# Optimization experiments

Measured on AMD Instinct MI355X. Metric: run time of the kernel, lower is better.

The kernel has to match this reference:

```python
import jax, jax.numpy as jnp
import numpy as np

DT = 5e-05
NUM_SUBSTEPS = 100
SPRING_Y = 30000.0
DASHPOT_DAMPING = 100.0
DRAG_DAMPING = 1.0
N_VERTICES = 100000
N_SPRINGS = 1000000


def setup_inputs() -> dict:
    key = jax.random.key(0)
    k1, k2, k3, k4 = jax.random.split(key, 4)
    x = jax.random.normal(k1, (N_VERTICES, 3), dtype=jnp.float32)
    x = x.at[:, 2].add(3.0)  # start mostly above the ground plane z=0
    # spring endpoints, guaranteed distinct so rest length / norm is never 0
    idx1 = jax.random.randint(k2, (N_SPRINGS,), 0, N_VERTICES)
    off = jax.random.randint(k3, (N_SPRINGS,), 1, N_VERTICES)
    idx2 = (idx1 + off) % N_VERTICES
    springs = jnp.stack([idx1, idx2], axis=1).astype(jnp.int64)
    # rest lengths = initial spring lengths (realistic: starts near equilibrium)
    rest = jnp.linalg.norm(x[idx2] - x[idx1], axis=1).astype(jnp.float32)
    masses = jax.random.uniform(k4, (N_VERTICES,), jnp.float32, 0.5, 1.5)
    return {
        "init_vertices": x,
        "init_springs": springs,
        "init_rest_lengths": rest,
        "init_masses": masses,
    }


def reference(init_vertices, init_springs, init_rest_lengths, init_masses):
    idx1 = init_springs[:, 0]
    idx2 = init_springs[:, 1]
    masses = init_masses[:, None]                      # [V,1]
    rest = init_rest_lengths[:, None]                  # [S,1]
    gravity = jnp.array([0.0, 0.0, -9.8], dtype=init_vertices.dtype)
    drag = jnp.exp(jnp.asarray(-DT * DRAG_DAMPING, dtype=init_vertices.dtype))

    def substep(carry, _):
        x, v = carry
        dis = x[idx2] - x[idx1]                        # [S,3] gather
        length = jnp.linalg.norm(dis, axis=1, keepdims=True)
        d = dis / length                               # unit spring direction
        spring_f = SPRING_Y * (length / rest - 1.0) * d
        v_rel = jnp.sum((v[idx2] - v[idx1]) * d, axis=1, keepdims=True)
        f_pair = spring_f + DASHPOT_DAMPING * v_rel * d  # fused spring+dashpot
        forces = masses * gravity                      # [V,3]
        forces = forces.at[idx1].add(f_pair)           # scatter-add
        forces = forces.at[idx2].add(-f_pair)
        v = (v + DT * forces / masses) * drag          # explicit Euler + drag
        x = x + DT * v
        x = x.at[:, 2].set(jnp.maximum(x[:, 2], 0.0))  # ground clamp
        v = v.at[:, 2].set(jnp.where(x[:, 2] == 0.0, 0.0, v[:, 2]))
        return (x, v), None

    v0 = jnp.zeros_like(init_vertices)
    (x, v), _ = jax.lax.scan(substep, (init_vertices, v0), None, length=NUM_SUBSTEPS)
    return x
```

## Files before the change

kernel.cpp:

```cpp
#include <hip/hip_runtime.h>
#include <hip/hip_fp16.h>

#define DT 5e-5f
#define SPRING_Y 30000.0f
#define DASHPOT 100.0f
#define DRAG 0.9999500012499792f



__global__ void init_k(const float* __restrict__ x0, float4* __restrict__ xv,
                       int* __restrict__ deg, int nv) {
    int i = blockIdx.x * blockDim.x + threadIdx.x;
    if (i < nv) {
        xv[2 * i]     = make_float4(x0[3 * i], x0[3 * i + 1], x0[3 * i + 2], 0.0f);
        xv[2 * i + 1] = make_float4(0.0f, 0.0f, 0.0f, 0.0f);
        deg[i] = 0;
    }
}

__global__ void fill_sliced_k(const int2* __restrict__ springs,
                              const float* __restrict__ rest,
                              int* __restrict__ deg, unsigned* __restrict__ adj,
                              int ns, int nv, int S) {
    int b = blockIdx.x;
    int slice = b & 7;
    int s = (b >> 3) * blockDim.x + threadIdx.x;
    if (s >= ns) return;

    int lo = (int)(((long long)slice * nv) >> 3);
    int hi = (int)(((long long)(slice + 1) * nv) >> 3);

    int2 p = springs[s];
    unsigned h = __half_as_ushort(__float2half(1.0f / rest[s])) & 0x7fffu;
    if (p.x >= lo && p.x < hi) {
        int a = atomicAdd(&deg[p.x], 1);
        adj[p.x * S + a] = ((unsigned)p.y << 15) | h;
    }
    if (p.y >= lo && p.y < hi) {
        int c = atomicAdd(&deg[p.y], 1);
        adj[p.y * S + c] = ((unsigned)p.x << 15) | h;
    }
}


__device__ __forceinline__ void spring_accum(
        int par, unsigned e, float msk, float4 t1, float4 t2,
        const float4& xa, const float4& va,
        float& fx, float& fy, float& fz) {
    float invr = __uint_as_float(((e & 0x7fffu) << 13) + (112u << 23));
    float4 xb, u;
    xb.x = par ? t2.x : t1.x;
    xb.y = par ? t2.y : t1.y;
    xb.z = par ? t2.z : t1.z;
    u.x  = par ? t1.x : t2.x;
    u.y  = par ? t1.y : t2.y;
    u.z  = par ? t1.z : t2.z;
    float vbx = __shfl_xor(u.x, 1);
    float vby = __shfl_xor(u.y, 1);
    float vbz = __shfl_xor(u.z, 1);

    float dx = xb.x - xa.x, dy = xb.y - xa.y, dz = xb.z - xa.z;
    float len = sqrtf(dx * dx + dy * dy + dz * dz);
    float il = 1.0f / len;
    float ddx = dx * il, ddy = dy * il, ddz = dz * il;
    float vrel = (vbx - va.x) * ddx + (vby - va.y) * ddy + (vbz - va.z) * ddz;
    float coef = (SPRING_Y * (len * invr - 1.0f) + DASHPOT * vrel) * msk;
    fx += coef * ddx;
    fy += coef * ddy;
    fz += coef * ddz;
}

__global__ void __launch_bounds__(256) substep_k(
        const float4* __restrict__ xvin, float4* __restrict__ xvout,
        const unsigned* __restrict__ adj, const int* __restrict__ deg,
        const float* __restrict__ mass, int nv, int S,
        float* __restrict__ out) {
    int gid = blockIdx.x * blockDim.x + threadIdx.x;
    int vid = gid >> 3;
    int sub = gid & 7;
    if (vid >= nv) return;

    float4 xa = xvin[2 * vid];
    float4 va = xvin[2 * vid + 1];
    float m  = mass[vid];
    int d  = deg[vid];
    int s0 = vid * S;
    int last = s0 + d - 1;
    int par  = sub & 1;
    int base = sub & ~1;
    int niter = (d > base) ? ((d - base + 7) >> 3) : 0;
    int pf = s0 + base;

    float fx = 0.0f, fy = 0.0f, fz = 0.0f;

    for (int u = 0; u < niter; u += 2) {
        int pb0 = pf + 8 * u;
        int pb1 = pb0 + 8;
        unsigned eA0 = adj[min(pb0,     last)];
        unsigned eB0 = adj[min(pb0 + 1, last)];
        unsigned eA1 = adj[min(pb1,     last)];
        unsigned eB1 = adj[min(pb1 + 1, last)];
        int nA0 = (int)(eA0 >> 15), nB0 = (int)(eB0 >> 15);
        int nA1 = (int)(eA1 >> 15), nB1 = (int)(eB1 >> 15);

        float4 t10 = xvin[2 * nA0 + par];
        float4 t20 = xvin[2 * nB0 + (1 - par)];
        float4 t11 = xvin[2 * nA1 + par];
        float4 t21 = xvin[2 * nB1 + (1 - par)];

        {
            float msk = (pb0 + par <= last) ? 1.0f : 0.0f;
            spring_accum(par, par ? eB0 : eA0, msk, t10, t20, xa, va, fx, fy, fz);
        }
        {
            float msk = (pb1 + par <= last) ? 1.0f : 0.0f;
            spring_accum(par, par ? eB1 : eA1, msk, t11, t21, xa, va, fx, fy, fz);
        }
    }

    fx += __shfl_xor(fx, 1);
    fx += __shfl_xor(fx, 2);
    fx += __shfl_xor(fx, 4);
    fy += __shfl_xor(fy, 1);
    fy += __shfl_xor(fy, 2);
    fy += __shfl_xor(fy, 4);
    fz += __shfl_xor(fz, 1);
    fz += __shfl_xor(fz, 2);
    fz += __shfl_xor(fz, 4);

    if (sub == 0) {
        fz += m * (-9.8f);
        float invm = 1.0f / m;

        va.x = (va.x + DT * fx * invm) * DRAG;
        va.y = (va.y + DT * fy * invm) * DRAG;
        va.z = (va.z + DT * fz * invm) * DRAG;

        xa.x += DT * va.x;
        xa.y += DT * va.y;
        xa.z += DT * va.z;
        xa.z = fmaxf(xa.z, 0.0f);
        if (xa.z == 0.0f) va.z = 0.0f;

        xvout[2 * vid]     = xa;
        xvout[2 * vid + 1] = va;

        if (out) {
            out[3 * vid + 0] = xa.x;
            out[3 * vid + 1] = xa.y;
            out[3 * vid + 2] = xa.z;
        }
    }
}

extern "C" void kernel_launch(void* const* d_in, const int* in_sizes, int n_in,
                              void* d_out, int out_size, void* d_ws, size_t ws_size,
                              hipStream_t stream) {
    const float* x0      = (const float*)d_in[0];
    const int2*  springs = (const int2*)d_in[1];
    const float* rest    = (const float*)d_in[2];
    const float* mass    = (const float*)d_in[3];

    const int ns = in_sizes[2];
    const int nv = in_sizes[3];
    const int nb = (nv + 255) / 256;

    char* ws = (char*)d_ws;
    size_t o = 0;
    float4* xva   = (float4*)(ws + o); o += (size_t)nv * 32;
    float4* xvb   = (float4*)(ws + o); o += (size_t)nv * 32;
    int* deg      = (int*)(ws + o);    o += (((size_t)nv * 4 + 15) & ~15ull);
    unsigned* adj = (unsigned*)(ws + o);

    const int STRIDE = 64;

    dim3 blk(256);
    dim3 vgrid(nb);
    dim3 fgrid(8 * ((ns + 255) / 256));
    dim3 subgrid(((size_t)nv * 8 + 255) / 256);

    init_k<<<vgrid, blk, 0, stream>>>(x0, xva, deg, nv);
    fill_sliced_k<<<fgrid, blk, 0, stream>>>(springs, rest, deg, adj, ns, nv, STRIDE);

    const int NSUB = 100;
    float4* xi = xva;
    float4* xo = xvb;
    for (int t = 0; t < NSUB; ++t) {
        float* out = (t == NSUB - 1) ? (float*)d_out : nullptr;
        substep_k<<<subgrid, blk, 0, stream>>>(xi, xo, adj, deg, mass, nv, STRIDE, out);
        float4* tmp = xi; xi = xo; xo = tmp;
    }
}
```

Before: 1.818 ms.

## Sort vertices by degree via counting sort to balance substep waves

Adds a histogram, a serial scan and a scatter pass that build a permutation of vertices grouped by degree. The substep kernel then maps each 8-lane group to perm[g], so neighbouring groups in a wavefront have similar loop trip counts and waste less time on divergence. In exchange, vertex accesses to x/v/mass/deg become scattered instead of contiguous, and there is one more indirection load per vertex per substep.

Measured after the change: 2.661 ms. 46.4% more time.

```diff
diff --git a/kernel.cpp b/kernel.cpp
--- a/kernel.cpp
+++ b/kernel.cpp
@@ -5,17 +5,19 @@
 #define SPRING_Y 30000.0f
 #define DASHPOT 100.0f
 #define DRAG 0.9999500012499792f
+#define NSUB 100
 
 
 
 __global__ void init_k(const float* __restrict__ x0, float4* __restrict__ xv,
-                       int* __restrict__ deg, int nv) {
+                       int* __restrict__ deg, int* __restrict__ cnt, int nv) {
     int i = blockIdx.x * blockDim.x + threadIdx.x;
     if (i < nv) {
         xv[2 * i]     = make_float4(x0[3 * i], x0[3 * i + 1], x0[3 * i + 2], 0.0f);
         xv[2 * i + 1] = make_float4(0.0f, 0.0f, 0.0f, 0.0f);
         deg[i] = 0;
     }
+    if (i < 130) cnt[i] = 0;
 }
 
 __global__ void fill_sliced_k(const int2* __restrict__ springs,
@@ -42,24 +44,47 @@
     }
 }
 
+__global__ void hist_k(const int* __restrict__ deg, int* __restrict__ cnt, int nv) {
+    int v = blockIdx.x * blockDim.x + threadIdx.x;
+    if (v < nv) atomicAdd(&cnt[min(deg[v], 64)], 1);
+}
+
+__global__ void scan_k(int* __restrict__ cnt) {
+    if (blockIdx.x == 0 && threadIdx.x == 0) {
+        int run = 0;
+        for (int i = 0; i <= 64; ++i) {
+            cnt[65 + i] = run;
+            run += cnt[i];
+        }
+    }
+}
+
+__global__ void scatter_k(const int* __restrict__ deg, int* __restrict__ cnt,
+                          int* __restrict__ perm, int nv) {
+    int v = blockIdx.x * blockDim.x + threadIdx.x;
+    if (v >= nv) return;
+    int b = min(deg[v], 64);
+    int pos = atomicAdd(&cnt[65 + b], 1);
+    perm[pos] = v;
+}
+
 
 __device__ __forceinline__ void spring_accum(
         int par, unsigned e, float msk, float4 t1, float4 t2,
         const float4& xa, const float4& va,
         float& fx, float& fy, float& fz) {
     float invr = __uint_as_float(((e & 0x7fffu) << 13) + (112u << 23));
-    float4 xb, u;
-    xb.x = par ? t2.x : t1.x;
-    xb.y = par ? t2.y : t1.y;
-    xb.z = par ? t2.z : t1.z;
-    u.x  = par ? t1.x : t2.x;
-    u.y  = par ? t1.y : t2.y;
-    u.z  = par ? t1.z : t2.z;
-    float vbx = __shfl_xor(u.x, 1);
-    float vby = __shfl_xor(u.y, 1);
-    float vbz = __shfl_xor(u.z, 1);
-
-    float dx = xb.x - xa.x, dy = xb.y - xa.y, dz = xb.z - xa.z;
+    float xbx = par ? t2.x : t1.x;
+    float xby = par ? t2.y : t1.y;
+    float xbz = par ? t2.z : t1.z;
+    float ux  = par ? t1.x : t2.x;
+    float uy  = par ? t1.y : t2.y;
+    float uz  = par ? t1.z : t2.z;
+    float vbx = __shfl_xor(ux, 1);
+    float vby = __shfl_xor(uy, 1);
+    float vbz = __shfl_xor(uz, 1);
+
+    float dx = xbx - xa.x, dy = xby - xa.y, dz = xbz - xa.z;
     float len = sqrtf(dx * dx + dy * dy + dz * dz);
     float il = 1.0f / len;
     float ddx = dx * il, ddy = dy * il, ddz = dz * il;
@@ -73,17 +98,19 @@
 __global__ void __launch_bounds__(256) substep_k(
         const float4* __restrict__ xvin, float4* __restrict__ xvout,
         const unsigned* __restrict__ adj, const int* __restrict__ deg,
+        const int* __restrict__ perm,
         const float* __restrict__ mass, int nv, int S,
         float* __restrict__ out) {
     int gid = blockIdx.x * blockDim.x + threadIdx.x;
-    int vid = gid >> 3;
+    int g   = gid >> 3;
     int sub = gid & 7;
-    if (vid >= nv) return;
+    if (g >= nv) return;
+    int vid = perm[g];
 
     float4 xa = xvin[2 * vid];
     float4 va = xvin[2 * vid + 1];
-    float m  = mass[vid];
-    int d  = deg[vid];
+    float m = mass[vid];
+    int d = deg[vid];
     int s0 = vid * S;
     int last = s0 + d - 1;
     int par  = sub & 1;
@@ -170,6 +197,9 @@
     float4* xva   = (float4*)(ws + o); o += (size_t)nv * 32;
     float4* xvb   = (float4*)(ws + o); o += (size_t)nv * 32;
     int* deg      = (int*)(ws + o);    o += (((size_t)nv * 4 + 15) & ~15ull);
+    int* perm     = (int*)(ws + o);    o += (((size_t)nv * 4 + 15) & ~15ull);
+    int* cnt      = (int*)(ws + o);    o += 130 * 4 + 8;
+    o = (o + 15) & ~15ull;
     unsigned* adj = (unsigned*)(ws + o);
 
     const int STRIDE = 64;
@@ -179,15 +209,18 @@
     dim3 fgrid(8 * ((ns + 255) / 256));
     dim3 subgrid(((size_t)nv * 8 + 255) / 256);
 
-    init_k<<<vgrid, blk, 0, stream>>>(x0, xva, deg, nv);
+    init_k<<<vgrid, blk, 0, stream>>>(x0, xva, deg, cnt, nv);
     fill_sliced_k<<<fgrid, blk, 0, stream>>>(springs, rest, deg, adj, ns, nv, STRIDE);
-
-    const int NSUB = 100;
+    hist_k<<<vgrid, blk, 0, stream>>>(deg, cnt, nv);
+    scan_k<<<dim3(1), dim3(64), 0, stream>>>(cnt);
+    scatter_k<<<vgrid, blk, 0, stream>>>(deg, cnt, perm, nv);
+
     float4* xi = xva;
     float4* xo = xvb;
     for (int t = 0; t < NSUB; ++t) {
         float* out = (t == NSUB - 1) ? (float*)d_out : nullptr;
-        substep_k<<<subgrid, blk, 0, stream>>>(xi, xo, adj, deg, mass, nv, STRIDE, out);
+        substep_k<<<subgrid, blk, 0, stream>>>(xi, xo, adj, deg, perm, mass, nv,
+                                               STRIDE, out);
         float4* tmp = xi; xi = xo; xo = tmp;
     }
 }
```

## Replace fixed-stride padded adjacency with compact CSR built by count-scan-place

Applied to the files above, without the earlier changes.

Replaces the fixed 64-slot-per-vertex adjacency array with a compact CSR layout. Degrees are counted first, then a three-kernel prefix scan yields row starts, and a sliced placement kernel fills the entries. Dense rows cut wasted cache lines and memory footprint in the 100 substep gathers, at the cost of a few extra setup kernels and a serial block-sum scan. It also removes the silent overflow risk when a vertex has more than 64 springs.

Measured after the change: 1.869 ms. +2.8%, slower.

```diff
diff --git a/kernel.cpp b/kernel.cpp
--- a/kernel.cpp
+++ b/kernel.cpp
@@ -5,6 +5,7 @@
 #define SPRING_Y 30000.0f
 #define DASHPOT 100.0f
 #define DRAG 0.9999500012499792f
+#define NSUB 100
 
 
 
@@ -18,10 +19,54 @@
     }
 }
 
-__global__ void fill_sliced_k(const int2* __restrict__ springs,
-                              const float* __restrict__ rest,
-                              int* __restrict__ deg, unsigned* __restrict__ adj,
-                              int ns, int nv, int S) {
+__global__ void count_k(const int2* __restrict__ springs, int* __restrict__ deg,
+                        int ns) {
+    int s = blockIdx.x * blockDim.x + threadIdx.x;
+    if (s >= ns) return;
+    int2 p = springs[s];
+    atomicAdd(&deg[p.x], 1);
+    atomicAdd(&deg[p.y], 1);
+}
+
+__global__ void scan1_k(const int* __restrict__ deg, int* __restrict__ rowstart,
+                        int* __restrict__ bsum, int nv) {
+    __shared__ int sh[256];
+    int t = threadIdx.x;
+    int i = blockIdx.x * 256 + t;
+    int v = (i < nv) ? deg[i] : 0;
+    sh[t] = v;
+    __syncthreads();
+    for (int off = 1; off < 256; off <<= 1) {
+        int add = (t >= off) ? sh[t - off] : 0;
+        __syncthreads();
+        sh[t] += add;
+        __syncthreads();
+    }
+    if (i < nv) rowstart[i] = sh[t] - v;
+    if (t == 255) bsum[blockIdx.x] = sh[255];
+}
+
+__global__ void scan2_k(int* __restrict__ bsum, int nb) {
+    if (blockIdx.x == 0 && threadIdx.x == 0) {
+        int run = 0;
+        for (int i = 0; i < nb; ++i) { int x = bsum[i]; bsum[i] = run; run += x; }
+    }
+}
+
+__global__ void scan3_k(int* __restrict__ rowstart, const int* __restrict__ bsum,
+                        int* __restrict__ cursor, int nv) {
+    int i = blockIdx.x * blockDim.x + threadIdx.x;
+    if (i < nv) {
+        int r = rowstart[i] + bsum[blockIdx.x];
+        rowstart[i] = r;
+        cursor[i]   = r;
+    }
+}
+
+__global__ void place_sliced_k(const int2* __restrict__ springs,
+                               const float* __restrict__ rest,
+                               int* __restrict__ cursor, unsigned* __restrict__ csr,
+                               int ns, int nv) {
     int b = blockIdx.x;
     int slice = b & 7;
     int s = (b >> 3) * blockDim.x + threadIdx.x;
@@ -32,14 +77,10 @@
 
     int2 p = springs[s];
     unsigned h = __half_as_ushort(__float2half(1.0f / rest[s])) & 0x7fffu;
-    if (p.x >= lo && p.x < hi) {
-        int a = atomicAdd(&deg[p.x], 1);
-        adj[p.x * S + a] = ((unsigned)p.y << 15) | h;
-    }
-    if (p.y >= lo && p.y < hi) {
-        int c = atomicAdd(&deg[p.y], 1);
-        adj[p.y * S + c] = ((unsigned)p.x << 15) | h;
-    }
+    if (p.x >= lo && p.x < hi)
+        csr[atomicAdd(&cursor[p.x], 1)] = ((unsigned)p.y << 15) | h;
+    if (p.y >= lo && p.y < hi)
+        csr[atomicAdd(&cursor[p.y], 1)] = ((unsigned)p.x << 15) | h;
 }
 
 
@@ -48,18 +89,17 @@
         const float4& xa, const float4& va,
         float& fx, float& fy, float& fz) {
     float invr = __uint_as_float(((e & 0x7fffu) << 13) + (112u << 23));
-    float4 xb, u;
-    xb.x = par ? t2.x : t1.x;
-    xb.y = par ? t2.y : t1.y;
-    xb.z = par ? t2.z : t1.z;
-    u.x  = par ? t1.x : t2.x;
-    u.y  = par ? t1.y : t2.y;
-    u.z  = par ? t1.z : t2.z;
-    float vbx = __shfl_xor(u.x, 1);
-    float vby = __shfl_xor(u.y, 1);
-    float vbz = __shfl_xor(u.z, 1);
-
-    float dx = xb.x - xa.x, dy = xb.y - xa.y, dz = xb.z - xa.z;
+    float xbx = par ? t2.x : t1.x;
+    float xby = par ? t2.y : t1.y;
+    float xbz = par ? t2.z : t1.z;
+    float ux  = par ? t1.x : t2.x;
+    float uy  = par ? t1.y : t2.y;
+    float uz  = par ? t1.z : t2.z;
+    float vbx = __shfl_xor(ux, 1);
+    float vby = __shfl_xor(uy, 1);
+    float vbz = __shfl_xor(uz, 1);
+
+    float dx = xbx - xa.x, dy = xby - xa.y, dz = xbz - xa.z;
     float len = sqrtf(dx * dx + dy * dy + dz * dz);
     float il = 1.0f / len;
     float ddx = dx * il, ddy = dy * il, ddz = dz * il;
@@ -73,7 +113,8 @@
 __global__ void __launch_bounds__(256) substep_k(
         const float4* __restrict__ xvin, float4* __restrict__ xvout,
         const unsigned* __restrict__ adj, const int* __restrict__ deg,
-        const float* __restrict__ mass, int nv, int S,
+        const int* __restrict__ rowstart,
+        const float* __restrict__ mass, int nv,
         float* __restrict__ out) {
     int gid = blockIdx.x * blockDim.x + threadIdx.x;
     int vid = gid >> 3;
@@ -82,9 +123,9 @@
 
     float4 xa = xvin[2 * vid];
     float4 va = xvin[2 * vid + 1];
-    float m  = mass[vid];
+    float m = mass[vid];
     int d  = deg[vid];
-    int s0 = vid * S;
+    int s0 = rowstart[vid];
     int last = s0 + d - 1;
     int par  = sub & 1;
     int base = sub & ~1;
@@ -170,24 +211,30 @@
     float4* xva   = (float4*)(ws + o); o += (size_t)nv * 32;
     float4* xvb   = (float4*)(ws + o); o += (size_t)nv * 32;
     int* deg      = (int*)(ws + o);    o += (((size_t)nv * 4 + 15) & ~15ull);
-    unsigned* adj = (unsigned*)(ws + o);
-
-    const int STRIDE = 64;
+    int* rowstart = (int*)(ws + o);    o += (((size_t)nv * 4 + 15) & ~15ull);
+    int* cursor   = (int*)(ws + o);    o += (((size_t)nv * 4 + 15) & ~15ull);
+    int* bsum     = (int*)(ws + o);    o += 512 * 4;
+    unsigned* csr = (unsigned*)(ws + o);
 
     dim3 blk(256);
     dim3 vgrid(nb);
-    dim3 fgrid(8 * ((ns + 255) / 256));
+    dim3 sgrid((ns + 255) / 256);
+    dim3 pgrid(8 * ((ns + 255) / 256));
     dim3 subgrid(((size_t)nv * 8 + 255) / 256);
 
     init_k<<<vgrid, blk, 0, stream>>>(x0, xva, deg, nv);
-    fill_sliced_k<<<fgrid, blk, 0, stream>>>(springs, rest, deg, adj, ns, nv, STRIDE);
-
-    const int NSUB = 100;
+    count_k<<<sgrid, blk, 0, stream>>>(springs, deg, ns);
+    scan1_k<<<vgrid, blk, 0, stream>>>(deg, rowstart, bsum, nv);
+    scan2_k<<<dim3(1), dim3(64), 0, stream>>>(bsum, nb);
+    scan3_k<<<vgrid, blk, 0, stream>>>(rowstart, bsum, cursor, nv);
+    place_sliced_k<<<pgrid, blk, 0, stream>>>(springs, rest, cursor, csr, ns, nv);
+
     float4* xi = xva;
     float4* xo = xvb;
     for (int t = 0; t < NSUB; ++t) {
         float* out = (t == NSUB - 1) ? (float*)d_out : nullptr;
-        substep_k<<<subgrid, blk, 0, stream>>>(xi, xo, adj, deg, mass, nv, STRIDE, out);
+        substep_k<<<subgrid, blk, 0, stream>>>(xi, xo, csr, deg, rowstart,
+                                               mass, nv, out);
         float4* tmp = xi; xi = xo; xo = tmp;
     }
 }
```
